# Performance work log

Measured on AMD Instinct MI355X. Metric: run time of the kernel, lower is better.

Reference implementation:

```python
import jax, jax.numpy as jnp
import numpy as np


def _attn(x, Wq, Wk, Wv, Wo, bo, heads):
    # x: [b, n, d] -> multi-head self-attention along n
    b, n, d = x.shape
    dh = d // heads
    q = (x @ Wq).reshape(b, n, heads, dh)
    k = (x @ Wk).reshape(b, n, heads, dh)
    v = (x @ Wv).reshape(b, n, heads, dh)
    scores = jnp.einsum('bnhd,bmhd->bhnm', q, k) * (dh ** -0.5)
    a = jax.nn.softmax(scores, axis=-1)
    o = jnp.einsum('bhnm,bmhd->bnhd', a, v).reshape(b, n, d)
    return o @ Wo + bo


def setup_inputs() -> dict:
    key = jax.random.key(0)
    ks = jax.random.split(key, 16)
    B, C, H, W, heads = 4, 128, 128, 128, 8
    s = 0.02
    inp = {
        'x': jax.random.normal(ks[0], (B, C, H, W), dtype=jnp.float32),
        'pos_h': jax.random.normal(ks[1], (1, C, H, 1), dtype=jnp.float32) * s,
        'pos_w': jax.random.normal(ks[2], (1, C, 1, W), dtype=jnp.float32) * s,
        'Wq_h': jax.random.normal(ks[3], (C, C), dtype=jnp.float32) * s,
        'Wk_h': jax.random.normal(ks[4], (C, C), dtype=jnp.float32) * s,
        'Wv_h': jax.random.normal(ks[5], (C, C), dtype=jnp.float32) * s,
        'Wo_h': jax.random.normal(ks[6], (C, C), dtype=jnp.float32) * s,
        'bo_h': jnp.zeros((C,), dtype=jnp.float32),
        'Wq_w': jax.random.normal(ks[7], (C, C), dtype=jnp.float32) * s,
        'Wk_w': jax.random.normal(ks[8], (C, C), dtype=jnp.float32) * s,
        'Wv_w': jax.random.normal(ks[9], (C, C), dtype=jnp.float32) * s,
        'Wo_w': jax.random.normal(ks[10], (C, C), dtype=jnp.float32) * s,
        'bo_w': jnp.zeros((C,), dtype=jnp.float32),
        'heads': heads,
    }
    return inp


def reference(x, pos_h, pos_w, Wq_h, Wk_h, Wv_h, Wo_h, bo_h, Wq_w, Wk_w, Wv_w, Wo_w, bo_w, heads):
    # x: [B, C, H, W] (dim_index=1). Axial positional embeddings added first.
    xp = x + pos_h + pos_w
    B, C, H, W = xp.shape
    # attention along H (rows): fold W into batch
    xh = jnp.transpose(xp, (0, 3, 2, 1)).reshape(B * W, H, C)
    oh = _attn(xh, Wq_h, Wk_h, Wv_h, Wo_h, bo_h, heads)
    oh = jnp.transpose(oh.reshape(B, W, H, C), (0, 3, 2, 1))
    # attention along W (cols): fold H into batch
    xw = jnp.transpose(xp, (0, 2, 3, 1)).reshape(B * H, W, C)
    ow = _attn(xw, Wq_w, Wk_w, Wv_w, Wo_w, bo_w, heads)
    ow = jnp.transpose(ow.reshape(B, H, W, C), (0, 3, 1, 2))
    # sum of axial outputs + outer residual
    return oh + ow + x
```

## Files before the change

kernel.cpp:

```cpp
#include <hip/hip_runtime.h>
#include <stdint.h>


typedef __attribute__((ext_vector_type(8))) short short8;
typedef __attribute__((ext_vector_type(4))) short short4_;
typedef __attribute__((ext_vector_type(4))) float f32x4;

#define DEVFN static __device__ __forceinline__

DEVFN uint16_t f2bf(float f) {
  uint32_t u = __builtin_bit_cast(uint32_t, f);
  u = (u + 0x7FFFu + ((u >> 16) & 1u)) >> 16;
  return (uint16_t)u;
}
DEVFN float bf2f(uint16_t h) {
  uint32_t u = ((uint32_t)h) << 16;
  return __builtin_bit_cast(float, u);
}
DEVFN uint32_t sw(int row, int boff) {
  return (uint32_t)((row << 8) | (boff ^ ((row & 7) << 4)));
}

__global__ __launch_bounds__(512) void k_prep(
    const float* __restrict__ x, const float* __restrict__ ph, const float* __restrict__ pw,
    const float* __restrict__ w0, const float* __restrict__ w1, const float* __restrict__ w2,
    const float* __restrict__ w3, const float* __restrict__ w4, const float* __restrict__ w5,
    const float* __restrict__ w6, const float* __restrict__ w7,
    uint16_t* __restrict__ xh, uint16_t* __restrict__ xw, uint16_t* __restrict__ wt)
{
  __shared__ float T[128 * 133];
  int bid = blockIdx.x, t = threadIdx.x;
  if (bid < 512) {
    int b = bid >> 7, h = bid & 127;
    const float* xb = x + ((size_t)b * 128) * 16384 + h * 128;
    #pragma unroll
    for (int p = 0; p < 8; ++p) {
      int c = (t >> 5) + (p << 4);
      int w0i = (t & 31) << 2;
      f32x4 xv = *(const f32x4*)(xb + (size_t)c * 16384 + w0i);
      float phv = ph[c * 128 + h];
      f32x4 pwv = *(const f32x4*)(pw + c * 128 + w0i);
      #pragma unroll
      for (int j = 0; j < 4; ++j) T[c * 133 + w0i + j] = xv[j] + phv + pwv[j];
    }
    __syncthreads();
    #pragma unroll
    for (int p = 0; p < 16; ++p) {
      int c2 = (t & 63) << 1;
      int w = (t >> 6) + (p << 3);
      float a0 = T[c2 * 133 + w], a1 = T[(c2 + 1) * 133 + w];
      uint32_t pk = (uint32_t)f2bf(a0) | ((uint32_t)f2bf(a1) << 16);
      size_t ih = ((((size_t)b * 128 + w) * 128 + h) * 128 + c2) >> 1;
      size_t iw = ((((size_t)b * 128 + h) * 128 + w) * 128 + c2) >> 1;
      ((uint32_t*)xh)[ih] = pk;
      ((uint32_t*)xw)[iw] = pk;
    }
  } else {
    int m = bid - 512;
    const float* Ws;
    switch (m) {
      case 0: Ws = w0; break; case 1: Ws = w1; break; case 2: Ws = w2; break;
      case 3: Ws = w3; break; case 4: Ws = w4; break; case 5: Ws = w5; break;
      case 6: Ws = w6; break; default: Ws = w7; break;
    }
    uint16_t* dst = wt + m * 16384;
    #pragma unroll
    for (int p = 0; p < 8; ++p) {
      int in = (t >> 5) + (p << 4);
      int o0 = (t & 31) << 2;
      f32x4 wv = *(const f32x4*)(Ws + in * 128 + o0);
      #pragma unroll
      for (int j = 0; j < 4; ++j) dst[(o0 + j) * 128 + in] = f2bf(wv[j]);
    }
  }
}

__global__ __launch_bounds__(512) void k_attn(
    const uint16_t* __restrict__ wt, uint16_t* __restrict__ xh, uint16_t* __restrict__ xw,
    const float* __restrict__ bo_h, const float* __restrict__ bo_w)
{
  __shared__ uint16_t sm[81920];
  uint16_t* Xb = sm;
  uint16_t* Qb = sm + 16384;
  uint16_t* Kb = sm + 32768;
  uint16_t* Vt = sm + 49152;
  uint16_t* Ab = sm + 65536;

  int bid = blockIdx.x;
  int dir = bid >> 9, sid = bid & 511;
  uint16_t* xbuf = (dir ? xw : xh) + (size_t)sid * 16384;
  const uint16_t* Wq = wt + dir * 65536;
  const uint16_t* Wk = Wq + 16384;
  const uint16_t* Wv = Wq + 32768;
  const uint16_t* Wo = Wq + 49152;
  const float* bo = dir ? bo_w : bo_h;

  int t = threadIdx.x, l = t & 63, wid = t >> 6, band = wid << 4;
  int lr = l & 15, lg = l >> 4;
  const f32x4 zf = {0.f, 0.f, 0.f, 0.f};

  #pragma unroll
  for (int i = 0; i < 4; ++i) {
    int fb = ((i << 9) | t) << 4;
    int row = fb >> 8, off = fb & 255;
    short8 v = *(const short8*)((const char*)xbuf + fb);
    *(short8*)((char*)Xb + sw(row, off)) = v;
  }
  __syncthreads();

  short8 ax[4];
  {
    int ar = band | lr;
    #pragma unroll
    for (int kt = 0; kt < 4; ++kt)
      ax[kt] = *(const short8*)((const char*)Xb + sw(ar, (kt << 6) | (lg << 4)));
  }

  #pragma unroll 1
  for (int pj = 0; pj < 3; ++pj) {
    const uint16_t* Wp = (pj == 0) ? Wq : (pj == 1) ? Wk : Wv;
    #pragma unroll 1
    for (int tc = 0; tc < 8; ++tc) {
      f32x4 acc = zf;
      int wr = (tc << 4) | lr;
      #pragma unroll
      for (int kt = 0; kt < 4; ++kt) {
        short8 bf = *(const short8*)((const char*)Wp + (wr << 8) + (kt << 6) + (lg << 4));
        acc = __builtin_amdgcn_mfma_f32_16x16x32_bf16(ax[kt], bf, acc, 0, 0, 0);
      }
      if (pj < 2) {
        uint16_t* dst = pj ? Kb : Qb;
        #pragma unroll
        for (int j = 0; j < 4; ++j) {
          int row = band + (lg << 2) + j;
          *(uint16_t*)((char*)dst + sw(row, wr << 1)) = f2bf(acc[j]);
        }
      } else {
        int r0 = band + (lg << 2);
        short4_ pk;
        pk[0] = (short)f2bf(acc[0]); pk[1] = (short)f2bf(acc[1]);
        pk[2] = (short)f2bf(acc[2]); pk[3] = (short)f2bf(acc[3]);
        *(short4_*)((char*)Vt + sw(wr, r0 << 1)) = pk;
      }
    }
  }
  __syncthreads();

  #pragma unroll 1
  for (int h = 0; h < 8; ++h) {
    int hb = h << 5;
    short8 aq = {0,0,0,0,0,0,0,0};
    if (l < 32) aq = *(const short8*)((const char*)Qb + sw(band | lr, hb | (lg << 4)));
    f32x4 s[8];
    #pragma unroll
    for (int tc = 0; tc < 8; ++tc) {
      short8 bk = {0,0,0,0,0,0,0,0};
      if (l < 32) bk = *(const short8*)((const char*)Kb + sw((tc << 4) | lr, hb | (lg << 4)));
      s[tc] = __builtin_amdgcn_mfma_f32_16x16x32_bf16(aq, bk, zf, 0, 0, 0);
    }
    #pragma unroll
    for (int j = 0; j < 4; ++j) {
      float mj = -1e30f;
      #pragma unroll
      for (int tc = 0; tc < 8; ++tc) { s[tc][j] *= 0.25f; mj = fmaxf(mj, s[tc][j]); }
      mj = fmaxf(mj, __shfl_xor(mj, 1));
      mj = fmaxf(mj, __shfl_xor(mj, 2));
      mj = fmaxf(mj, __shfl_xor(mj, 4));
      mj = fmaxf(mj, __shfl_xor(mj, 8));
      float sum = 0.f;
      #pragma unroll
      for (int tc = 0; tc < 8; ++tc) { float e = __expf(s[tc][j] - mj); s[tc][j] = e; sum += e; }
      sum += __shfl_xor(sum, 1);
      sum += __shfl_xor(sum, 2);
      sum += __shfl_xor(sum, 4);
      sum += __shfl_xor(sum, 8);
      float r = __builtin_amdgcn_rcpf(sum);
      int row = band + (lg << 2) + j;
      #pragma unroll
      for (int tc = 0; tc < 8; ++tc)
        *(uint16_t*)((char*)Ab + sw(row, ((tc << 4) | lr) << 1)) = f2bf(s[tc][j] * r);
    }
    asm volatile("s_waitcnt lgkmcnt(0)" ::: "memory");
    f32x4 acco = zf;
    #pragma unroll
    for (int kt = 0; kt < 4; ++kt) {
      short8 pa = *(const short8*)((const char*)Ab + sw(band | lr, (kt << 6) | (lg << 4)));
      short8 bv = *(const short8*)((const char*)Vt + sw((h << 4) | lr, (kt << 6) | (lg << 4)));
      acco = __builtin_amdgcn_mfma_f32_16x16x32_bf16(pa, bv, acco, 0, 0, 0);
    }
    int col = (h << 4) | lr;
    #pragma unroll
    for (int j = 0; j < 4; ++j) {
      int row = band + (lg << 2) + j;
      *(uint16_t*)((char*)Xb + sw(row, col << 1)) = f2bf(acco[j]);
    }
  }
  asm volatile("s_waitcnt lgkmcnt(0)" ::: "memory");

  short8 ao[4];
  {
    int ar = band | lr;
    #pragma unroll
    for (int kt = 0; kt < 4; ++kt)
      ao[kt] = *(const short8*)((const char*)Xb + sw(ar, (kt << 6) | (lg << 4)));
  }
  #pragma unroll 1
  for (int tc = 0; tc < 8; ++tc) {
    f32x4 acc = zf;
    int wr = (tc << 4) | lr;
    #pragma unroll
    for (int kt = 0; kt < 4; ++kt) {
      short8 bf = *(const short8*)((const char*)Wo + (wr << 8) + (kt << 6) + (lg << 4));
      acc = __builtin_amdgcn_mfma_f32_16x16x32_bf16(ao[kt], bf, acc, 0, 0, 0);
    }
    float bov = bo[wr];
    #pragma unroll
    for (int j = 0; j < 4; ++j) {
      int row = band + (lg << 2) + j;
      *(uint16_t*)((char*)Qb + sw(row, wr << 1)) = f2bf(acc[j] + bov);
    }
  }
  asm volatile("s_waitcnt lgkmcnt(0)" ::: "memory");
  #pragma unroll
  for (int p = 0; p < 4; ++p) {
    int fb = (p << 10) | (l << 4);
    int row = band + (fb >> 8), off = fb & 255;
    short8 v = *(const short8*)((const char*)Qb + sw(row, off));
    *(short8*)((char*)xbuf + (row << 8) + off) = v;
  }
}

__global__ __launch_bounds__(512) void k_comb(
    const uint16_t* __restrict__ xh, const uint16_t* __restrict__ xw,
    const float* __restrict__ x, float* __restrict__ out)
{
  __shared__ float T[128 * 133];
  int bid = blockIdx.x, t = threadIdx.x;
  int b = bid >> 7, h = bid & 127;
  #pragma unroll 1
  for (int p = 0; p < 16; ++p) {
    int c2 = (t & 63) << 1;
    int w = (t >> 6) + (p << 3);
    uint32_t o2 = *(const uint32_t*)(xh + ((((size_t)b * 128 + w) * 128 + h) * 128 + c2));
    uint32_t y2 = *(const uint32_t*)(xw + ((((size_t)b * 128 + h) * 128 + w) * 128 + c2));
    T[c2 * 133 + w]       = bf2f((uint16_t)o2) + bf2f((uint16_t)y2);
    T[(c2 + 1) * 133 + w] = bf2f((uint16_t)(o2 >> 16)) + bf2f((uint16_t)(y2 >> 16));
  }
  __syncthreads();
  #pragma unroll 1
  for (int p = 0; p < 8; ++p) {
    int c = (t >> 5) + (p << 4);
    int w0i = (t & 31) << 2;
    size_t xi = ((size_t)b * 128 + c) * 16384 + (size_t)h * 128 + w0i;
    f32x4 xv = *(const f32x4*)(x + xi);
    f32x4 o;
    #pragma unroll
    for (int j = 0; j < 4; ++j) o[j] = T[c * 133 + w0i + j] + xv[j];
    *(f32x4*)(out + xi) = o;
  }
}

extern "C" void kernel_launch(void* const* d_in, const int* in_sizes, int n_in,
                              void* d_out, int out_size, void* d_ws, size_t ws_size,
                              hipStream_t stream) {
  const float* x    = (const float*)d_in[0];
  const float* ph   = (const float*)d_in[1];
  const float* pw   = (const float*)d_in[2];
  const float* Wq_h = (const float*)d_in[3];
  const float* Wk_h = (const float*)d_in[4];
  const float* Wv_h = (const float*)d_in[5];
  const float* Wo_h = (const float*)d_in[6];
  const float* bo_h = (const float*)d_in[7];
  const float* Wq_w = (const float*)d_in[8];
  const float* Wk_w = (const float*)d_in[9];
  const float* Wv_w = (const float*)d_in[10];
  const float* Wo_w = (const float*)d_in[11];
  const float* bo_w = (const float*)d_in[12];
  float* out = (float*)d_out;

  uint16_t* xh = (uint16_t*)d_ws;
  uint16_t* xw = xh + 8388608;
  uint16_t* wt = xw + 8388608;

  k_prep<<<520, 512, 0, stream>>>(x, ph, pw, Wq_h, Wk_h, Wv_h, Wo_h,
                                  Wq_w, Wk_w, Wv_w, Wo_w, xh, xw, wt);
  k_attn<<<1024, 512, 0, stream>>>(wt, xh, xw, bo_h, bo_w);
  k_comb<<<512, 512, 0, stream>>>(xh, xw, x, out);
}
```

Before: 321.5 us.

## Keep Q, probabilities and head outputs in registers, fuse Wo projection per head

```diff
diff --git a/kernel.cpp b/kernel.cpp
--- a/kernel.cpp
+++ b/kernel.cpp
@@ -3,7 +3,7 @@
 
 
 typedef __attribute__((ext_vector_type(8))) short short8;
-typedef __attribute__((ext_vector_type(4))) short short4_;
+typedef __attribute__((ext_vector_type(4))) short bf16x4;
 typedef __attribute__((ext_vector_type(4))) float f32x4;
 
 #define DEVFN static __device__ __forceinline__
@@ -17,8 +17,26 @@
   uint32_t u = ((uint32_t)h) << 16;
   return __builtin_bit_cast(float, u);
 }
-DEVFN uint32_t sw(int row, int boff) {
-  return (uint32_t)((row << 8) | (boff ^ ((row & 7) << 4)));
+DEVFN bf16x4 pack4(float a0, float a1, float a2, float a3) {
+  bf16x4 r;
+  r[0] = (short)f2bf(a0);
+  r[1] = (short)f2bf(a1);
+  r[2] = (short)f2bf(a2);
+  r[3] = (short)f2bf(a3);
+  return r;
+}
+
+DEVFN f32x4 mfma16(bf16x4 a, bf16x4 b, f32x4 c) {
+#if __has_builtin(__builtin_amdgcn_mfma_f32_16x16x16bf16_1k)
+  return __builtin_amdgcn_mfma_f32_16x16x16bf16_1k(a, b, c, 0, 0, 0);
+#elif __has_builtin(__builtin_amdgcn_mfma_f32_16x16x16_bf16)
+  return __builtin_amdgcn_mfma_f32_16x16x16_bf16(a, b, c, 0, 0, 0);
+#else
+  f32x4 d;
+  asm volatile("s_nop 1\n\tv_mfma_f32_16x16x16_bf16 %0, %1, %2, %3\n\ts_nop 7\n\ts_nop 7"
+               : "=v"(d) : "v"(a), "v"(b), "v"(c));
+  return d;
+#endif
 }
 
 __global__ __launch_bounds__(512) void k_prep(
@@ -75,158 +93,125 @@
   }
 }
 
-__global__ __launch_bounds__(512) void k_attn(
+__global__ __launch_bounds__(512, 4) void k_attn(
     const uint16_t* __restrict__ wt, uint16_t* __restrict__ xh, uint16_t* __restrict__ xw,
     const float* __restrict__ bo_h, const float* __restrict__ bo_w)
 {
-  __shared__ uint16_t sm[81920];
-  uint16_t* Xb = sm;
-  uint16_t* Qb = sm + 16384;
-  uint16_t* Kb = sm + 32768;
-  uint16_t* Vt = sm + 49152;
-  uint16_t* Ab = sm + 65536;
+  __shared__ uint16_t sm[32768];
+  uint16_t* Kb = sm;
+  uint16_t* Vt = sm + 16384;
 
   int bid = blockIdx.x;
   int dir = bid >> 9, sid = bid & 511;
   uint16_t* xbuf = (dir ? xw : xh) + (size_t)sid * 16384;
-  const uint16_t* Wq = wt + dir * 65536;
-  const uint16_t* Wk = Wq + 16384;
-  const uint16_t* Wv = Wq + 32768;
-  const uint16_t* Wo = Wq + 49152;
+  const char* Wq = (const char*)(wt + dir * 65536);
+  const char* Wk = Wq + 32768;
+  const char* Wv = Wq + 65536;
+  const char* Wo = Wq + 98304;
   const float* bo = dir ? bo_w : bo_h;
 
-  int t = threadIdx.x, l = t & 63, wid = t >> 6, band = wid << 4;
+  int t = threadIdx.x, l = t & 63, band = (t >> 6) << 4;
   int lr = l & 15, lg = l >> 4;
+  int swz = (lr & 7) << 4;
   const f32x4 zf = {0.f, 0.f, 0.f, 0.f};
-
-  #pragma unroll
-  for (int i = 0; i < 4; ++i) {
-    int fb = ((i << 9) | t) << 4;
-    int row = fb >> 8, off = fb & 255;
-    short8 v = *(const short8*)((const char*)xbuf + fb);
-    *(short8*)((char*)Xb + sw(row, off)) = v;
-  }
-  __syncthreads();
 
   short8 ax[4];
   {
-    int ar = band | lr;
+    const char* xr = (const char*)xbuf + ((band + lr) << 8) + (lg << 4);
+    ax[0] = *(const short8*)(xr);
+    ax[1] = *(const short8*)(xr + 64);
+    ax[2] = *(const short8*)(xr + 128);
+    ax[3] = *(const short8*)(xr + 192);
+  }
+
+  bf16x4 qf[8];
+  const float cs = 0.36067376022f;
+
+  #pragma unroll 2
+  for (int tc = 0; tc < 8; ++tc) {
+    f32x4 a = zf;
+    const char* wb = Wq + (((tc << 4) | lr) << 8) + (lg << 4);
     #pragma unroll
     for (int kt = 0; kt < 4; ++kt)
-      ax[kt] = *(const short8*)((const char*)Xb + sw(ar, (kt << 6) | (lg << 4)));
-  }
-
-  #pragma unroll 1
-  for (int pj = 0; pj < 3; ++pj) {
-    const uint16_t* Wp = (pj == 0) ? Wq : (pj == 1) ? Wk : Wv;
-    #pragma unroll 1
-    for (int tc = 0; tc < 8; ++tc) {
-      f32x4 acc = zf;
-      int wr = (tc << 4) | lr;
-      #pragma unroll
-      for (int kt = 0; kt < 4; ++kt) {
-        short8 bf = *(const short8*)((const char*)Wp + (wr << 8) + (kt << 6) + (lg << 4));
-        acc = __builtin_amdgcn_mfma_f32_16x16x32_bf16(ax[kt], bf, acc, 0, 0, 0);
-      }
-      if (pj < 2) {
-        uint16_t* dst = pj ? Kb : Qb;
-        #pragma unroll
-        for (int j = 0; j < 4; ++j) {
-          int row = band + (lg << 2) + j;
-          *(uint16_t*)((char*)dst + sw(row, wr << 1)) = f2bf(acc[j]);
-        }
-      } else {
-        int r0 = band + (lg << 2);
-        short4_ pk;
-        pk[0] = (short)f2bf(acc[0]); pk[1] = (short)f2bf(acc[1]);
-        pk[2] = (short)f2bf(acc[2]); pk[3] = (short)f2bf(acc[3]);
-        *(short4_*)((char*)Vt + sw(wr, r0 << 1)) = pk;
-      }
-    }
+      a = __builtin_amdgcn_mfma_f32_16x16x32_bf16(*(const short8*)(wb + (kt << 6)), ax[kt], a, 0, 0, 0);
+    qf[tc] = pack4(a[0] * cs, a[1] * cs, a[2] * cs, a[3] * cs);
+  }
+  #pragma unroll 2
+  for (int tc = 0; tc < 8; ++tc) {
+    f32x4 a = zf;
+    const char* wb = Wk + (((tc << 4) | lr) << 8) + (lg << 4);
+    #pragma unroll
+    for (int kt = 0; kt < 4; ++kt)
+      a = __builtin_amdgcn_mfma_f32_16x16x32_bf16(*(const short8*)(wb + (kt << 6)), ax[kt], a, 0, 0, 0);
+    *(bf16x4*)((char*)Kb + ((band + lr) << 8) + (((tc << 5) | (lg << 3)) ^ swz)) =
+        pack4(a[0], a[1], a[2], a[3]);
+  }
+  #pragma unroll 2
+  for (int tc = 0; tc < 8; ++tc) {
+    f32x4 a = zf;
+    const char* wb = Wv + (((tc << 4) | lr) << 8) + (lg << 4);
+    #pragma unroll
+    for (int kt = 0; kt < 4; ++kt)
+      a = __builtin_amdgcn_mfma_f32_16x16x32_bf16(ax[kt], *(const short8*)(wb + (kt << 6)), a, 0, 0, 0);
+    *(bf16x4*)((char*)Vt + (((tc << 4) | lr) << 8) + (((band << 1) | (lg << 3)) ^ swz)) =
+        pack4(a[0], a[1], a[2], a[3]);
   }
   __syncthreads();
+
+  f32x4 y[8];
+  #pragma unroll
+  for (int tc = 0; tc < 8; ++tc) y[tc] = zf;
 
   #pragma unroll 1
   for (int h = 0; h < 8; ++h) {
-    int hb = h << 5;
-    short8 aq = {0,0,0,0,0,0,0,0};
-    if (l < 32) aq = *(const short8*)((const char*)Qb + sw(band | lr, hb | (lg << 4)));
     f32x4 s[8];
     #pragma unroll
+    for (int tt = 0; tt < 8; ++tt) {
+      bf16x4 kf = *(const bf16x4*)((const char*)Kb + (((tt << 4) | lr) << 8) +
+                                   (((h << 5) | (lg << 3)) ^ swz));
+      s[tt] = mfma16(kf, qf[h], zf);
+    }
+    float mx = -3.0e38f;
+    #pragma unroll
+    for (int tt = 0; tt < 8; ++tt)
+      #pragma unroll
+      for (int j = 0; j < 4; ++j) mx = fmaxf(mx, s[tt][j]);
+    mx = fmaxf(mx, __shfl_xor(mx, 16));
+    mx = fmaxf(mx, __shfl_xor(mx, 32));
+    float sum = 0.f;
+    #pragma unroll
+    for (int tt = 0; tt < 8; ++tt)
+      #pragma unroll
+      for (int j = 0; j < 4; ++j) {
+        float p = __builtin_amdgcn_exp2f(s[tt][j] - mx);
+        s[tt][j] = p; sum += p;
+      }
+    sum += __shfl_xor(sum, 16);
+    sum += __shfl_xor(sum, 32);
+
+    f32x4 o = zf;
+    #pragma unroll
+    for (int tt = 0; tt < 8; ++tt) {
+      bf16x4 pt = pack4(s[tt][0], s[tt][1], s[tt][2], s[tt][3]);
+      bf16x4 vf = *(const bf16x4*)((const char*)Vt + (((h << 4) | lr) << 8) +
+                                   (((tt << 5) | (lg << 3)) ^ swz));
+      o = mfma16(vf, pt, o);
+    }
+    float r = __builtin_amdgcn_rcpf(sum);
+    bf16x4 ob = pack4(o[0] * r, o[1] * r, o[2] * r, o[3] * r);
+
+    #pragma unroll
     for (int tc = 0; tc < 8; ++tc) {
-      short8 bk = {0,0,0,0,0,0,0,0};
-      if (l < 32) bk = *(const short8*)((const char*)Kb + sw((tc << 4) | lr, hb | (lg << 4)));
-      s[tc] = __builtin_amdgcn_mfma_f32_16x16x32_bf16(aq, bk, zf, 0, 0, 0);
-    }
-    #pragma unroll
-    for (int j = 0; j < 4; ++j) {
-      float mj = -1e30f;
-      #pragma unroll
-      for (int tc = 0; tc < 8; ++tc) { s[tc][j] *= 0.25f; mj = fmaxf(mj, s[tc][j]); }
-      mj = fmaxf(mj, __shfl_xor(mj, 1));
-      mj = fmaxf(mj, __shfl_xor(mj, 2));
-      mj = fmaxf(mj, __shfl_xor(mj, 4));
-      mj = fmaxf(mj, __shfl_xor(mj, 8));
-      float sum = 0.f;
-      #pragma unroll
-      for (int tc = 0; tc < 8; ++tc) { float e = __expf(s[tc][j] - mj); s[tc][j] = e; sum += e; }
-      sum += __shfl_xor(sum, 1);
-      sum += __shfl_xor(sum, 2);
-      sum += __shfl_xor(sum, 4);
-      sum += __shfl_xor(sum, 8);
-      float r = __builtin_amdgcn_rcpf(sum);
-      int row = band + (lg << 2) + j;
-      #pragma unroll
-      for (int tc = 0; tc < 8; ++tc)
-        *(uint16_t*)((char*)Ab + sw(row, ((tc << 4) | lr) << 1)) = f2bf(s[tc][j] * r);
-    }
-    asm volatile("s_waitcnt lgkmcnt(0)" ::: "memory");
-    f32x4 acco = zf;
-    #pragma unroll
-    for (int kt = 0; kt < 4; ++kt) {
-      short8 pa = *(const short8*)((const char*)Ab + sw(band | lr, (kt << 6) | (lg << 4)));
-      short8 bv = *(const short8*)((const char*)Vt + sw((h << 4) | lr, (kt << 6) | (lg << 4)));
-      acco = __builtin_amdgcn_mfma_f32_16x16x32_bf16(pa, bv, acco, 0, 0, 0);
-    }
-    int col = (h << 4) | lr;
-    #pragma unroll
-    for (int j = 0; j < 4; ++j) {
-      int row = band + (lg << 2) + j;
-      *(uint16_t*)((char*)Xb + sw(row, col << 1)) = f2bf(acco[j]);
-    }
-  }
-  asm volatile("s_waitcnt lgkmcnt(0)" ::: "memory");
-
-  short8 ao[4];
-  {
-    int ar = band | lr;
-    #pragma unroll
-    for (int kt = 0; kt < 4; ++kt)
-      ao[kt] = *(const short8*)((const char*)Xb + sw(ar, (kt << 6) | (lg << 4)));
-  }
-  #pragma unroll 1
-  for (int tc = 0; tc < 8; ++tc) {
-    f32x4 acc = zf;
-    int wr = (tc << 4) | lr;
-    #pragma unroll
-    for (int kt = 0; kt < 4; ++kt) {
-      short8 bf = *(const short8*)((const char*)Wo + (wr << 8) + (kt << 6) + (lg << 4));
-      acc = __builtin_amdgcn_mfma_f32_16x16x32_bf16(ao[kt], bf, acc, 0, 0, 0);
-    }
-    float bov = bo[wr];
-    #pragma unroll
-    for (int j = 0; j < 4; ++j) {
-      int row = band + (lg << 2) + j;
-      *(uint16_t*)((char*)Qb + sw(row, wr << 1)) = f2bf(acc[j] + bov);
-    }
-  }
-  asm volatile("s_waitcnt lgkmcnt(0)" ::: "memory");
+      bf16x4 wf = *(const bf16x4*)(Wo + (((tc << 4) | lr) << 8) + (h << 5) + (lg << 3));
+      y[tc] = mfma16(wf, ob, y[tc]);
+    }
+  }
+
   #pragma unroll
-  for (int p = 0; p < 4; ++p) {
-    int fb = (p << 10) | (l << 4);
-    int row = band + (fb >> 8), off = fb & 255;
-    short8 v = *(const short8*)((const char*)Qb + sw(row, off));
-    *(short8*)((char*)xbuf + (row << 8) + off) = v;
+  for (int tc = 0; tc < 8; ++tc) {
+    f32x4 bv = *(const f32x4*)(bo + (tc << 4) + (lg << 2));
+    *(bf16x4*)((char*)xbuf + ((band + lr) << 8) + (tc << 5) + (lg << 3)) =
+        pack4(y[tc][0] + bv[0], y[tc][1] + bv[1], y[tc][2] + bv[2], y[tc][3] + bv[3]);
   }
 }
 
```

Result: faster. 305.1 us (-5.1%).
